# Optimization experiments

Measured on AMD Instinct MI355X. Metric: run time of the kernel, lower is better.

The kernel has to match this reference:

```python
import jax, jax.numpy as jnp
import numpy as np

EPS = 1e-5

def conv1x1(x, w, b):
    # x: [B,Cin,H,W], w: [Cout,Cin], b: [Cout]
    return jnp.einsum('oi,bihw->bohw', w, x) + b[None, :, None, None]

def self_attention(x, qw, qb, kw, kb, vw, vb, fw, fb):
    B, C, H, W = x.shape
    hid = qw.shape[0]
    q = conv1x1(x, qw, qb).reshape(B, hid, H * W).transpose(0, 2, 1)   # [B,HW,hid]
    k = conv1x1(x, kw, kb).reshape(B, hid, H * W)                      # [B,hid,HW]
    v = conv1x1(x, vw, vb).reshape(B, C, H * W)                        # [B,C,HW]
    attn = jax.nn.softmax(jnp.einsum('bnh,bhm->bnm', q, k), axis=-1)   # [B,HW,HW]
    z = jnp.einsum('bnm,bcm->bnc', attn, v)                            # [B,HW,C]
    # faithful to torch .view(B,C,H,W) on contiguous [B,HW,C]: raw reshape, no transpose
    z = z.reshape(B, C, H, W)
    return conv1x1(z * x, fw, fb) + x

def group_norm_per_channel(y, gw, gb):
    # GroupNorm(num_groups == num_channels): per-channel instance norm, biased var
    mean = y.mean(axis=(2, 3), keepdims=True)
    var = ((y - mean) ** 2).mean(axis=(2, 3), keepdims=True)
    yn = (y - mean) * jax.lax.rsqrt(var + EPS)
    return yn * gw[None, :, None, None] + gb[None, :, None, None]

def setup_inputs() -> dict:
    key = jax.random.key(0)
    ks = jax.random.split(key, 32)
    B, C, H, W = 4, 64, 64, 64
    hid, att = 64, 64
    d = {}
    d['x'] = jax.random.normal(ks[0], (B, C, H, W), jnp.float32)
    d['h'] = jax.random.normal(ks[1], (B, hid, H, W), jnp.float32)
    d['c'] = jax.random.normal(ks[2], (B, hid, H, W), jnp.float32)
    i = 3
    for pre, cin in (('ax', C), ('ah', hid)):
        for nm, cout in (('q', att), ('k', att), ('v', cin), ('f', cin)):
            d[f'{pre}_{nm}w'] = jax.random.normal(ks[i], (cout, cin), jnp.float32) * 0.05; i += 1
            d[f'{pre}_{nm}b'] = jax.random.normal(ks[i], (cout,), jnp.float32) * 0.05; i += 1
    d['conv_w'] = jax.random.normal(ks[i], (4 * hid, C + hid, 3, 3), jnp.float32) * 0.05; i += 1
    d['conv_b'] = jax.random.normal(ks[i], (4 * hid,), jnp.float32) * 0.05; i += 1
    d['gn_w'] = jnp.ones((4 * hid,), jnp.float32)
    d['gn_b'] = jnp.zeros((4 * hid,), jnp.float32)
    return d

def reference(x, h, c,
              ax_qw, ax_qb, ax_kw, ax_kb, ax_vw, ax_vb, ax_fw, ax_fb,
              ah_qw, ah_qb, ah_kw, ah_kb, ah_vw, ah_vb, ah_fw, ah_fb,
              conv_w, conv_b, gn_w, gn_b):
    hid = h.shape[1]
    xa = self_attention(x, ax_qw, ax_qb, ax_kw, ax_kb, ax_vw, ax_vb, ax_fw, ax_fb)
    ha = self_attention(h, ah_qw, ah_qb, ah_kw, ah_kb, ah_vw, ah_vb, ah_fw, ah_fb)
    combined = jnp.concatenate([xa, ha], axis=1)
    y = jax.lax.conv_general_dilated(
        combined, conv_w, window_strides=(1, 1), padding=[(1, 1), (1, 1)],
        dimension_numbers=('NCHW', 'OIHW', 'NCHW')) + conv_b[None, :, None, None]
    y = group_norm_per_channel(y, gn_w, gn_b)
    i, f, o, g = jnp.split(y, 4, axis=1)
    i = jax.nn.sigmoid(i); f = jax.nn.sigmoid(f); o = jax.nn.sigmoid(o); g = jnp.tanh(g)
    c_next = f * c + i * g
    h_next = o * jnp.tanh(c_next)
    return jnp.stack([h_next, c_next])  # [2,B,hid,H,W]
```

## Files before the change

kernel.cpp:

```cpp
#include <hip/hip_runtime.h>
#include <hip/hip_bf16.h>


typedef __hip_bfloat16 bf16;
typedef const __hip_bfloat16* bfp;
typedef short bf16x8 __attribute__((ext_vector_type(8)));
typedef short short4v __attribute__((ext_vector_type(4)));
typedef float f32x4 __attribute__((ext_vector_type(4)));
typedef float f32x16 __attribute__((ext_vector_type(16)));
typedef unsigned int u32x4 __attribute__((ext_vector_type(4)));

#define SM_SHIFT 12.0f
#define SM_A  184.66496523378733f
#define SM_B  14034.452417194552f

__device__ __forceinline__ float ldf(const void* p, long i, int f32) {
    return f32 ? ((const float*)p)[i]
               : __bfloat162float(((const bf16*)p)[i]);
}
__device__ __forceinline__ short f2bf(float f) {
    bf16 h = __float2bfloat16(f);
    return *reinterpret_cast<short*>(&h);
}
__device__ __forceinline__ float bfv(short s) {
    unsigned short u = (unsigned short)s;
    return __bfloat162float(*reinterpret_cast<const bf16*>(&u));
}

__device__ __forceinline__ int sniff_f32(const void* xr)
{
    int lane = threadIdx.x & 63;
    unsigned long long v = ((const unsigned long long*)xr)[lane];
    int ok = 0;
#pragma unroll
    for (int i = 0; i < 4; ++i) {
        int e = (int)((v >> (16 * i + 7)) & 0xFF);
        ok += (e >= 100 && e <= 141);
    }
    ok += __shfl_xor(ok, 1, 64);
    ok += __shfl_xor(ok, 2, 64);
    ok += __shfl_xor(ok, 4, 64);
    ok += __shfl_xor(ok, 8, 64);
    ok += __shfl_xor(ok, 16, 64);
    ok += __shfl_xor(ok, 32, 64);
    return ok < 200;
}

__global__ __launch_bounds__(256) void qkv_kernel(
    const void* __restrict__ Xx, const void* __restrict__ Xh,
    const void* __restrict__ qwx, const void* __restrict__ qbx,
    const void* __restrict__ kwx, const void* __restrict__ kbx,
    const void* __restrict__ vwx, const void* __restrict__ vbx,
    const void* __restrict__ qwh, const void* __restrict__ qbh,
    const void* __restrict__ kwh, const void* __restrict__ kbh,
    const void* __restrict__ vwh, const void* __restrict__ vbh,
    bf16* __restrict__ Qx, bf16* __restrict__ Kx, bf16* __restrict__ Vtx,
    bf16* __restrict__ Qh, bf16* __restrict__ Kh, bf16* __restrict__ Vth,
    const void* __restrict__ cw, bf16* __restrict__ Wt,
    float* __restrict__ gacc, int qkvN)
{
    int bx = blockIdx.x;
    int tid = threadIdx.x;
    int f32 = sniff_f32(Xx);
    if (bx >= qkvN) {
        if (bx == qkvN) {
            for (int j = 0; j < 8; ++j)
                gacc[tid * 8 + j] = 0.f;
        }
        int wi = (bx - qkvN) * 256 + tid;
        int tap = wi >> 15;
        int rem = wi & 32767;
        int oc = rem >> 7, ic = rem & 127;
        Wt[wi] = __float2bfloat16(ldf(cw, ((long)oc * 128 + ic) * 9 + tap, f32));
        return;
    }
    __shared__ __align__(16) short xt[64][72];
    __shared__ __align__(16) short wq[64][72];
    __shared__ __align__(16) short wk[64][72];
    __shared__ __align__(16) short wv[64][72];
    int ab  = (bx >> 8) & 1;
    int idx = bx & 255;
    int b = idx >> 6;
    int n0 = (idx & 63) * 64;
    int wave = tid >> 6, lane = tid & 63;
    int q = lane >> 4, l15 = lane & 15;

    const void* X = ab ? Xh : Xx;
    const void* qw = ab ? qwh : qwx; const void* qb = ab ? qbh : qbx;
    const void* kw = ab ? kwh : kwx; const void* kb = ab ? kbh : kbx;
    const void* vw = ab ? vwh : vwx; const void* vb = ab ? vbh : vbx;
    short* Qg  = (short*)(ab ? Qh  : Qx)  + (long)b * 262144;
    short* Kg  = (short*)(ab ? Kh  : Kx)  + (long)b * 262144;
    short* Vtg = (short*)(ab ? Vth : Vtx) + (long)b * 262144;

    if (!f32) {
        const short* q16 = (const short*)qw;
        const short* k16 = (const short*)kw;
        const short* v16 = (const short*)vw;
        for (int rep = 0; rep < 2; ++rep) {
            int j8 = (rep * 256 + tid) * 8;
            *(bf16x8*)&wq[j8 >> 6][j8 & 63] = *(const bf16x8*)(q16 + j8);
            *(bf16x8*)&wk[j8 >> 6][j8 & 63] = *(const bf16x8*)(k16 + j8);
            *(bf16x8*)&wv[j8 >> 6][j8 & 63] = *(const bf16x8*)(v16 + j8);
        }
    } else {
        for (int rep = 0; rep < 16; ++rep) {
            int j = rep * 256 + tid;
            int i = j >> 6, cc = j & 63;
            wq[i][cc] = f2bf(((const float*)qw)[j]);
            wk[i][cc] = f2bf(((const float*)kw)[j]);
            wv[i][cc] = f2bf(((const float*)vw)[j]);
        }
    }
    long xbase = (long)b * 262144;
    if (!f32) {
        const short* X16 = (const short*)X;
        for (int rep = 0; rep < 2; ++rep) {
            int c = rep * 32 + (tid >> 3);
            int p8 = (tid & 7) * 8;
            bf16x8 v = *(const bf16x8*)(X16 + xbase + (long)c * 4096 + n0 + p8);
#pragma unroll
            for (int j = 0; j < 8; ++j) xt[p8 + j][c] = v[j];
        }
    } else {
        for (int rep = 0; rep < 16; ++rep) {
            int c = rep * 4 + (tid >> 6);
            int p = tid & 63;
            xt[p][c] = f2bf(ldf(X, xbase + (long)c * 4096 + n0 + p, f32));
        }
    }
    __syncthreads();

    bf16x8 a0 = *(const bf16x8*)&xt[wave * 16 + l15][q * 8];
    bf16x8 a1 = *(const bf16x8*)&xt[wave * 16 + l15][32 + q * 8];

    for (int ct = 0; ct < 4; ++ct) {
        bf16x8 bq0 = *(const bf16x8*)&wq[ct * 16 + l15][q * 8];
        bf16x8 bq1 = *(const bf16x8*)&wq[ct * 16 + l15][32 + q * 8];
        f32x4 z = (f32x4){0.f, 0.f, 0.f, 0.f};
        z = __builtin_amdgcn_mfma_f32_16x16x32_bf16(a0, bq0, z, 0, 0, 0);
        z = __builtin_amdgcn_mfma_f32_16x16x32_bf16(a1, bq1, z, 0, 0, 0);
        float bias = ldf(qb, ct * 16 + l15, f32);
        for (int reg = 0; reg < 4; ++reg)
            Qg[(long)(n0 + wave * 16 + q * 4 + reg) * 64 + ct * 16 + l15] =
                f2bf(z[reg] + bias);
    }
    for (int ct = 0; ct < 4; ++ct) {
        bf16x8 bk0 = *(const bf16x8*)&wk[ct * 16 + l15][q * 8];
        bf16x8 bk1 = *(const bf16x8*)&wk[ct * 16 + l15][32 + q * 8];
        f32x4 z = (f32x4){0.f, 0.f, 0.f, 0.f};
        z = __builtin_amdgcn_mfma_f32_16x16x32_bf16(a0, bk0, z, 0, 0, 0);
        z = __builtin_amdgcn_mfma_f32_16x16x32_bf16(a1, bk1, z, 0, 0, 0);
        float bias = ldf(kb, ct * 16 + l15, f32);
        for (int reg = 0; reg < 4; ++reg)
            Kg[(long)(n0 + wave * 16 + q * 4 + reg) * 64 + ct * 16 + l15] =
                f2bf(z[reg] + bias);
    }
    bf16x8 av0 = *(const bf16x8*)&wv[wave * 16 + l15][q * 8];
    bf16x8 av1 = *(const bf16x8*)&wv[wave * 16 + l15][32 + q * 8];
    for (int ct = 0; ct < 4; ++ct) {
        bf16x8 bx0 = *(const bf16x8*)&xt[ct * 16 + l15][q * 8];
        bf16x8 bx1 = *(const bf16x8*)&xt[ct * 16 + l15][32 + q * 8];
        f32x4 z = (f32x4){0.f, 0.f, 0.f, 0.f};
        z = __builtin_amdgcn_mfma_f32_16x16x32_bf16(av0, bx0, z, 0, 0, 0);
        z = __builtin_amdgcn_mfma_f32_16x16x32_bf16(av1, bx1, z, 0, 0, 0);
        for (int reg = 0; reg < 4; ++reg) {
            int c_out = wave * 16 + q * 4 + reg;
            float bias = ldf(vb, c_out, f32);
            Vtg[(long)c_out * 4096 + n0 + ct * 16 + l15] = f2bf(z[reg] + bias);
        }
    }
}

__global__ __launch_bounds__(256, 2) void attn_kernel(
    bfp Qx, bfp Kx, bfp Vtx, bf16* Ox,
    bfp Qh, bfp Kh, bfp Vth, bf16* Oh,
    float* __restrict__ lw, int split)
{
    __shared__ __align__(16) short ks [2][64][64];
    __shared__ __align__(16) short vts[2][64][64];
    int tid = threadIdx.x;
    int wave = tid >> 6, lane = tid & 63;
    int l31 = lane & 31, hi = lane >> 5;
    int nh = wave >> 1, mh = wave & 1;
    int idx = blockIdx.x & 255;
    int ab, half, mstart, ntile;
    if (split) {
        ab = blockIdx.x >> 9; half = (blockIdx.x >> 8) & 1;
        mstart = half * 2048; ntile = 32;
    } else {
        ab = blockIdx.x >> 8; half = 0; mstart = 0; ntile = 64;
    }
    int b = idx >> 6;
    int rt = idx & 63;
    int n0b = rt * 64;
    const short* Qb  = (const short*)(ab ? Qh  : Qx)  + (long)b * 262144;
    const short* Kb  = (const short*)(ab ? Kh  : Kx)  + (long)b * 262144;
    const short* Vtb = (const short*)(ab ? Vth : Vtx) + (long)b * 262144;
    short* Ob = (short*)(ab ? Oh : Ox) + (long)half * (1l << 20) + (long)b * 262144;

    int nq = n0b + nh * 32 + l31;
    bf16x8 aq[4];
#pragma unroll
    for (int kc = 0; kc < 4; ++kc)
        aq[kc] = *(const bf16x8*)(Qb + (long)nq * 64 + kc * 16 + hi * 8);

    f32x16 acc0 = (f32x16)(0.0f);
    f32x16 acc1 = (f32x16)(0.0f);
    f32x16 acc_l = (f32x16)(0.0f);
    const short ONE = 0x3F80;
    const bf16x8 ones = {ONE, ONE, ONE, ONE, ONE, ONE, ONE, ONE};

    int sw = (l31 >> 1) & 7;

    int r0 = tid >> 3, r1 = r0 + 32;
    int g = tid & 7;
    int sr0 = (r0 & 51) | ((r0 & 4) << 1) | ((r0 & 8) >> 1);
    int sr1 = sr0 + 32;
    int gk = (g ^ ((sr0 >> 1) & 7)) << 3;
    int gv = (g ^ ((r0 >> 1) & 7)) << 3;

    bf16x8 pk0 = *(const bf16x8*)(Kb + (long)(mstart + r0) * 64 + g * 8);
    bf16x8 pk1 = *(const bf16x8*)(Kb + (long)(mstart + r1) * 64 + g * 8);
    bf16x8 pv0 = *(const bf16x8*)(Vtb + (long)r0 * 4096 + mstart + g * 8);
    bf16x8 pv1 = *(const bf16x8*)(Vtb + (long)r1 * 4096 + mstart + g * 8);

    for (int it = 0; it < ntile; ++it) {
        int buf = it & 1;
        *(bf16x8*)&ks[buf][sr0][gk] = pk0;
        *(bf16x8*)&ks[buf][sr1][gk] = pk1;
        *(bf16x8*)&vts[buf][r0][gv] = pv0;
        *(bf16x8*)&vts[buf][r1][gv] = pv1;
        __syncthreads();
        if (it + 1 < ntile) {
            long m = (long)mstart + (long)(it + 1) * 64;
            pk0 = *(const bf16x8*)(Kb + (m + r0) * 64 + g * 8);
            pk1 = *(const bf16x8*)(Kb + (m + r1) * 64 + g * 8);
            pv0 = *(const bf16x8*)(Vtb + (long)r0 * 4096 + m + g * 8);
            pv1 = *(const bf16x8*)(Vtb + (long)r1 * 4096 + m + g * 8);
        }

        f32x16 s = (f32x16)(0.0f);
        const short* kbase = &ks[buf][mh * 32 + l31][0];
#pragma unroll
        for (int kc = 0; kc < 4; ++kc) {
            bf16x8 ak = *(const bf16x8*)(kbase + (((kc * 2 + hi) ^ sw) << 3));
            s = __builtin_amdgcn_mfma_f32_32x32x16_bf16(ak, aq[kc], s, 0, 0, 0);
        }

        unsigned P32[8];
#pragma unroll
        for (int i = 0; i < 8; ++i) {
            unsigned b0 = (unsigned)fmaxf(fmaf(s[2 * i],     SM_A, SM_B), 0.f);
            unsigned b1 = (unsigned)fmaxf(fmaf(s[2 * i + 1], SM_A, SM_B), 0.f);
            P32[i] = b0 | (b1 << 16);
        }
        u32x4 B0v = (u32x4){P32[0], P32[1], P32[2], P32[3]};
        u32x4 B1v = (u32x4){P32[4], P32[5], P32[6], P32[7]};
        bf16x8 bp0 = __builtin_bit_cast(bf16x8, B0v);
        bf16x8 bp1 = __builtin_bit_cast(bf16x8, B1v);

        acc_l = __builtin_amdgcn_mfma_f32_32x32x16_bf16(ones, bp0, acc_l, 0, 0, 0);
        acc_l = __builtin_amdgcn_mfma_f32_32x32x16_bf16(ones, bp1, acc_l, 0, 0, 0);

        const short* v0base = &vts[buf][l31][0];
        const short* v1base = &vts[buf][32 + l31][0];
#pragma unroll
        for (int mc = 0; mc < 2; ++mc) {
            int gm = ((mh * 4 + mc * 2 + hi) ^ sw) << 3;
            bf16x8 av0 = *(const bf16x8*)(v0base + gm);
            bf16x8 av1 = *(const bf16x8*)(v1base + gm);
            bf16x8 bp = mc ? bp1 : bp0;
            acc0 = __builtin_amdgcn_mfma_f32_32x32x16_bf16(av0, bp, acc0, 0, 0, 0);
            acc1 = __builtin_amdgcn_mfma_f32_32x32x16_bf16(av1, bp, acc1, 0, 0, 0);
        }
    }

    float l_acc = acc_l[0];

    __syncthreads();
    float* fs = (float*)&ks[0][0][0];
    float* fl = fs + 4096;
    if (mh == 1) {
#pragma unroll
        for (int r = 0; r < 16; ++r) {
            int row = (r & 3) + ((r >> 2) << 3) + (hi << 2);
            fs[nh * 2048 + row * 32 + l31]        = acc0[r];
            fs[nh * 2048 + 1024 + row * 32 + l31] = acc1[r];
        }
        if (lane < 32) fl[nh * 32 + l31] = l_acc;
    }
    __syncthreads();
    if (mh == 0) {
        float l_tot = l_acc + fl[nh * 32 + l31];
#pragma unroll
        for (int r = 0; r < 16; ++r) {
            int row = (r & 3) + ((r >> 2) << 3) + (hi << 2);
            acc0[r] += fs[nh * 2048 + row * 32 + l31];
            acc1[r] += fs[nh * 2048 + 1024 + row * 32 + l31];
        }
        int n = n0b + nh * 32 + l31;
        short* dst = Ob + (long)n * 64;
        if (split) {
            if (lane < 32)
                lw[(long)ab * 32768 + (long)half * 16384
                   + (long)b * 4096 + n] = l_tot;
#pragma unroll
            for (int rq = 0; rq < 4; ++rq) {
                int c0 = (rq << 3) + (hi << 2);
                short4v o4a, o4b;
#pragma unroll
                for (int j = 0; j < 4; ++j) {
                    o4a[j] = f2bf(acc0[rq * 4 + j]);
                    o4b[j] = f2bf(acc1[rq * 4 + j]);
                }
                *(short4v*)(dst + c0)      = o4a;
                *(short4v*)(dst + 32 + c0) = o4b;
            }
        } else {
            float iln = 1.f / l_tot;
#pragma unroll
            for (int rq = 0; rq < 4; ++rq) {
                int c0 = (rq << 3) + (hi << 2);
                short4v o4a, o4b;
#pragma unroll
                for (int j = 0; j < 4; ++j) {
                    o4a[j] = f2bf(acc0[rq * 4 + j] * iln);
                    o4b[j] = f2bf(acc1[rq * 4 + j] * iln);
                }
                *(short4v*)(dst + c0)      = o4a;
                *(short4v*)(dst + 32 + c0) = o4b;
            }
        }
    }
}

__global__ __launch_bounds__(256) void attnout_kernel(
    bfp Ox, const void* __restrict__ Xx,
    const void* __restrict__ fwx, const void* __restrict__ fbx,
    bf16* __restrict__ outx,
    bfp Oh, const void* __restrict__ Xh,
    const void* __restrict__ fwh, const void* __restrict__ fbh,
    bf16* __restrict__ outh,
    const float* __restrict__ lw, int split)
{
    __shared__ __align__(16) short fwt[64][72];
    __shared__ __align__(16) short at [64][72];
    int f32 = sniff_f32(Xx);
    int ab  = blockIdx.x >> 8;
    int idx = blockIdx.x & 255;
    int b = idx >> 6;
    int h = idx & 63;
    int tid = threadIdx.x;
    int wave = tid >> 6, lane = tid & 63;
    int q = lane >> 4, l15 = lane & 15;
    bfp O = ab ? Oh : Ox;
    const void* X = ab ? Xh : Xx;
    const void* fw = ab ? fwh : fwx;
    const void* fb = ab ? fbh : fbx;
    bf16* out = ab ? outh : outx;

    if (!f32) {
        const short* f16p = (const short*)fw;
        for (int rep = 0; rep < 2; ++rep) {
            int j8 = (rep * 256 + tid) * 8;
            *(bf16x8*)&fwt[j8 >> 6][j8 & 63] = *(const bf16x8*)(f16p + j8);
        }
    } else {
        for (int rep = 0; rep < 16; ++rep) {
            int j = rep * 256 + tid;
            fwt[j >> 6][j & 63] = f2bf(((const float*)fw)[j]);
        }
    }
    const short* Ob0 = (const short*)(O + (long)b * 262144);
    const short* Ob1 = Ob0 + (1l << 20);
    const float* lp0 = lw + (long)ab * 32768 + (long)b * 4096;
    const float* lp1 = lp0 + 16384;
    long xbase = (long)b * 262144;
    {
        int cn = tid >> 3;
        int w8 = (tid & 7) * 8;
        for (int rep = 0; rep < 2; ++rep, cn += 32) {
            int n = cn * 64 + h;
            bf16x8 o0 = *(const bf16x8*)(Ob0 + (long)n * 64 + w8);
            float pr[8];
            if (split) {
                float il = 1.f / (lp0[n] + lp1[n]);
                bf16x8 o1 = *(const bf16x8*)(Ob1 + (long)n * 64 + w8);
#pragma unroll
                for (int j = 0; j < 8; ++j)
                    pr[j] = (bfv(o0[j]) + bfv(o1[j])) * il;
            } else {
#pragma unroll
                for (int j = 0; j < 8; ++j)
                    pr[j] = bfv(o0[j]);
            }
            if (!f32) {
                bf16x8 xv = *(const bf16x8*)(
                    (const short*)X + xbase + (long)cn * 4096 + h * 64 + w8);
#pragma unroll
                for (int j = 0; j < 8; ++j)
                    at[w8 + j][cn] = f2bf(pr[j] * bfv(xv[j]));
            } else {
#pragma unroll
                for (int j = 0; j < 8; ++j)
                    at[w8 + j][cn] = f2bf(pr[j] *
                        ((const float*)X)[xbase + (long)cn * 4096 + h * 64 + w8 + j]);
            }
        }
    }
    __syncthreads();
    bf16x8 a0 = *(const bf16x8*)&fwt[wave * 16 + l15][q * 8];
    bf16x8 a1 = *(const bf16x8*)&fwt[wave * 16 + l15][32 + q * 8];
    short* outp = (short*)out;
    for (int nt = 0; nt < 4; ++nt) {
        bf16x8 b0 = *(const bf16x8*)&at[nt * 16 + l15][q * 8];
        bf16x8 b1 = *(const bf16x8*)&at[nt * 16 + l15][32 + q * 8];
        f32x4 z = (f32x4){0.f, 0.f, 0.f, 0.f};
        z = __builtin_amdgcn_mfma_f32_16x16x32_bf16(a0, b0, z, 0, 0, 0);
        z = __builtin_amdgcn_mfma_f32_16x16x32_bf16(a1, b1, z, 0, 0, 0);
        int w = nt * 16 + l15;
        short4v o4;
        for (int reg = 0; reg < 4; ++reg) {
            int o = wave * 16 + q * 4 + reg;
            float v = z[reg] + ldf(fb, o, f32) +
                      ldf(X, xbase + (long)o * 4096 + h * 64 + w, f32);
            o4[reg] = f2bf(v);
        }
        *(short4v*)(outp + (((long)(b * 64 + h) * 64 + w) * 64 + wave * 16 + q * 4)) = o4;
    }
}

__global__ __launch_bounds__(256) void conv3x3_kernel(
    bfp xa, bfp ha, bfp Wt, const void* __restrict__ cb,
    bf16* __restrict__ y, float* __restrict__ gacc,
    const void* __restrict__ xraw)
{
    __shared__ __align__(16) short in_s[3][66][136];
    int f32 = sniff_f32(xraw);
    int bx = blockIdx.x;
    int b = bx >> 7;
    int rem = bx & 127;
    int h = rem >> 1;
    int halfoc = rem & 1;
    int tid = threadIdx.x;
    int wave = tid >> 6, lane = tid & 63;
    int q = lane >> 4, l15 = lane & 15;

    const short* xab = (const short*)xa + (long)b * 262144;
    const short* hab = (const short*)ha + (long)b * 262144;
    const bf16x8 zv = {0, 0, 0, 0, 0, 0, 0, 0};
    for (int r = 0; r < 3; ++r) {
        int gy = h + r - 1;
        bool valid = (gy >= 0) && (gy < 64);
        for (int s = 0; s < 2; ++s) {
            int strip = s * 256 + tid;
            int w = strip >> 3;
            int c8 = (strip & 7) * 8;
            bf16x8 vx = zv, vh = zv;
            if (valid) {
                vx = *(const bf16x8*)(xab + ((long)gy * 64 + w) * 64 + c8);
                vh = *(const bf16x8*)(hab + ((long)gy * 64 + w) * 64 + c8);
            }
            *(bf16x8*)&in_s[r][w + 1][c8]      = vx;
            *(bf16x8*)&in_s[r][w + 1][64 + c8] = vh;
        }
    }
    if (tid < 96) {
        int r = tid / 32;
        int rest = tid % 32;
        int col = (rest & 1) ? 65 : 0;
        int c8 = (rest >> 1) * 8;
        *(bf16x8*)&in_s[r][col][c8] = zv;
    }
    __syncthreads();

    int oc0 = halfoc * 128 + wave * 32;
    f32x4 acc[2][4];
    for (int mt = 0; mt < 2; ++mt)
        for (int nt = 0; nt < 4; ++nt)
            acc[mt][nt] = (f32x4){0.f, 0.f, 0.f, 0.f};

    const short* Wb = (const short*)Wt;
    for (int tap = 0; tap < 9; ++tap) {
        int dy = tap / 3, dx = tap - dy * 3;
        for (int kc = 0; kc < 4; ++kc) {
            bf16x8 afrag[2];
            for (int mt = 0; mt < 2; ++mt)
                afrag[mt] = *(const bf16x8*)(
                    Wb + ((long)tap * 256 + oc0 + mt * 16 + l15) * 128 + kc * 32 + q * 8);
            for (int nt = 0; nt < 4; ++nt) {
                bf16x8 bfrag = *(const bf16x8*)&in_s[dy][nt * 16 + l15 + dx][kc * 32 + q * 8];
                for (int mt = 0; mt < 2; ++mt)
                    acc[mt][nt] = __builtin_amdgcn_mfma_f32_16x16x32_bf16(
                        afrag[mt], bfrag, acc[mt][nt], 0, 0, 0);
            }
        }
    }

    long ybase = (long)b * 1048576 + (long)h * 64;
    for (int mt = 0; mt < 2; ++mt) {
        for (int reg = 0; reg < 4; ++reg) {
            int oc = oc0 + mt * 16 + q * 4 + reg;
            float bias = ldf(cb, oc, f32);
            float s = 0.f, s2 = 0.f;
            for (int nt = 0; nt < 4; ++nt) {
                float v = acc[mt][nt][reg] + bias;
                ((short*)y)[ybase + (long)oc * 4096 + nt * 16 + l15] = f2bf(v);
                s += v; s2 = fmaf(v, v, s2);
            }
            s  += __shfl_xor(s,  1, 64);  s2 += __shfl_xor(s2, 1, 64);
            s  += __shfl_xor(s,  2, 64);  s2 += __shfl_xor(s2, 2, 64);
            s  += __shfl_xor(s,  4, 64);  s2 += __shfl_xor(s2, 4, 64);
            s  += __shfl_xor(s,  8, 64);  s2 += __shfl_xor(s2, 8, 64);
            if (l15 == 0) {
                atomicAdd(&gacc[b * 256 + oc], s);
                atomicAdd(&gacc[1024 + b * 256 + oc], s2);
            }
        }
    }
}

__global__ __launch_bounds__(256) void gates_kernel(
    bfp y, const float* __restrict__ gacc,
    const void* __restrict__ gw, const void* __restrict__ gb,
    const void* __restrict__ c_in, void* __restrict__ out)
{
    int f32 = sniff_f32(c_in);
    int idx = blockIdx.x * 256 + threadIdx.x;
    int b = idx >> 18;
    int r = idx & 262143;
    int ch = r >> 12;
    int pix = r & 4095;
    long ybase = (long)b * 1048576;
    float vals[4];
    for (int g = 0; g < 4; ++g) {
        int cc = g * 64 + ch;
        float mu  = gacc[b * 256 + cc] * (1.f / 4096.f);
        float var = gacc[1024 + b * 256 + cc] * (1.f / 4096.f) - mu * mu;
        float rstd = rsqrtf(fmaxf(var, 0.f) + 1e-5f);
        float v = __bfloat162float(y[ybase + (long)cc * 4096 + pix]);
        v = (v - mu) * rstd * ldf(gw, cc, f32) + ldf(gb, cc, f32);
        vals[g] = v;
    }
    float ig = 1.f / (1.f + __expf(-vals[0]));
    float fg = 1.f / (1.f + __expf(-vals[1]));
    float og = 1.f / (1.f + __expf(-vals[2]));
    float gg = tanhf(vals[3]);
    float cprev = ldf(c_in, idx, f32);
    float cn = fg * cprev + ig * gg;
    float hn = og * tanhf(cn);
    if (f32) {
        float* o32 = (float*)out;
        o32[idx] = hn;
        o32[1048576 + idx] = cn;
    } else {
        bf16* o16 = (bf16*)out;
        o16[idx] = __float2bfloat16(hn);
        o16[1048576 + idx] = __float2bfloat16(cn);
    }
}

extern "C" void kernel_launch(void* const* d_in, const int* in_sizes, int n_in,
                              void* d_out, int out_size, void* d_ws, size_t ws_size,
                              hipStream_t stream)
{
    const void* x = d_in[0]; const void* h = d_in[1]; const void* c = d_in[2];
    const void* ax_qw = d_in[3],  *ax_qb = d_in[4];
    const void* ax_kw = d_in[5],  *ax_kb = d_in[6];
    const void* ax_vw = d_in[7],  *ax_vb = d_in[8];
    const void* ax_fw = d_in[9],  *ax_fb = d_in[10];
    const void* ah_qw = d_in[11], *ah_qb = d_in[12];
    const void* ah_kw = d_in[13], *ah_kb = d_in[14];
    const void* ah_vw = d_in[15], *ah_vb = d_in[16];
    const void* ah_fw = d_in[17], *ah_fb = d_in[18];
    const void* conv_w = d_in[19], *conv_b = d_in[20];
    const void* gn_w = d_in[21],  *gn_b = d_in[22];

    char* wsb = (char*)d_ws;
    auto S = [&](int i) { return wsb + ((unsigned long)i << 21); };
    bool splitm = ws_size >= (27ul << 20);
    bool fused  = splitm || ws_size >= (18ul << 20) + 16384;

    bf16* ha = (bf16*)S(0);
    bf16* Wt = (bf16*)S(1);
    bf16 *Qx, *Kx, *Vtx, *Qh, *Kh, *Vth, *xa, *y, *Ox, *Oh;
    char* tail;
    if (splitm) {
        Qx = (bf16*)S(2); Kx = (bf16*)S(3); Vtx = (bf16*)S(4);
        Qh = (bf16*)S(5); Kh = (bf16*)S(6); Vth = (bf16*)S(7);
        xa = (bf16*)S(8);
        Ox = (bf16*)S(9);
        Oh = (bf16*)S(11);
        y = Qx;
        tail = S(13);
    } else if (fused) {
        Qx = (bf16*)S(2); Kx = (bf16*)S(3); Vtx = (bf16*)S(4);
        Qh = (bf16*)S(5); Kh = (bf16*)S(6); Vth = (bf16*)S(7);
        xa = (bf16*)S(8); Ox = Qx; Oh = Qh; y = Qx;
        tail = S(9);
    } else {
        Qx = (bf16*)S(2); Kx = (bf16*)S(3); Vtx = (bf16*)S(4);
        Qh = Qx; Kh = Kx; Vth = Vtx;
        xa = (bf16*)S(6); Ox = Qx; Oh = Qh; y = Qx;
        tail = S(7);
    }
    float* gacc = (float*)tail;
    float* lw   = (float*)(tail + 8192);

    if (fused) {
        qkv_kernel<<<512 + 1152, 256, 0, stream>>>(
            x, h,
            ax_qw, ax_qb, ax_kw, ax_kb, ax_vw, ax_vb,
            ah_qw, ah_qb, ah_kw, ah_kb, ah_vw, ah_vb,
            Qx, Kx, Vtx, Qh, Kh, Vth, conv_w, Wt, gacc, 512);
        if (splitm) {
            attn_kernel<<<1024, 256, 0, stream>>>(
                Qx, Kx, Vtx, Ox, Qh, Kh, Vth, Oh, lw, 1);
            attnout_kernel<<<512, 256, 0, stream>>>(
                Ox, x, ax_fw, ax_fb, xa, Oh, h, ah_fw, ah_fb, ha, lw, 1);
        } else {
            attn_kernel<<<512, 256, 0, stream>>>(
                Qx, Kx, Vtx, Ox, Qh, Kh, Vth, Oh, lw, 0);
            attnout_kernel<<<512, 256, 0, stream>>>(
                Ox, x, ax_fw, ax_fb, xa, Oh, h, ah_fw, ah_fb, ha, lw, 0);
        }
    } else {
        qkv_kernel<<<256 + 1152, 256, 0, stream>>>(
            x, x,
            ax_qw, ax_qb, ax_kw, ax_kb, ax_vw, ax_vb,
            ax_qw, ax_qb, ax_kw, ax_kb, ax_vw, ax_vb,
            Qx, Kx, Vtx, Qx, Kx, Vtx, conv_w, Wt, gacc, 256);
        attn_kernel<<<256, 256, 0, stream>>>(
            Qx, Kx, Vtx, Ox, Qx, Kx, Vtx, Ox, lw, 0);
        attnout_kernel<<<256, 256, 0, stream>>>(
            Ox, x, ax_fw, ax_fb, xa, Ox, x, ax_fw, ax_fb, xa, lw, 0);
        qkv_kernel<<<256, 256, 0, stream>>>(
            h, h,
            ah_qw, ah_qb, ah_kw, ah_kb, ah_vw, ah_vb,
            ah_qw, ah_qb, ah_kw, ah_kb, ah_vw, ah_vb,
            Qh, Kh, Vth, Qh, Kh, Vth, conv_w, Wt, gacc, 256);
        attn_kernel<<<256, 256, 0, stream>>>(
            Qh, Kh, Vth, Oh, Qh, Kh, Vth, Oh, lw, 0);
        attnout_kernel<<<256, 256, 0, stream>>>(
            Oh, h, ah_fw, ah_fb, ha, Oh, h, ah_fw, ah_fb, ha, lw, 0);
    }
    conv3x3_kernel<<<512, 256, 0, stream>>>(xa, ha, Wt, conv_b, y, gacc, x);
    gates_kernel<<<4096, 256, 0, stream>>>(y, gacc, gn_w, gn_b, c, d_out);
}
```

Baseline: 205.3 us.

## Fuse attention output projection into attention kernel and vectorize gates kernel

The attention kernel now gathers each block's query rows as one spatial row (the n = c*64 + h mapping). It then applies the output 1x1 conv, the multiply by x and the residual in-kernel through LDS, so the separate attnout kernel and the intermediate O buffer round trip are gone. The split-M path with partial-sum workspace is removed, so attention always runs 512 blocks over the full key range. The gates kernel processes 8 pixels per thread with vector loads and stores. This saves one launch and global traffic, but drops the extra parallelism the split path gave and adds an epilogue tail to the attention blocks.

```diff
diff --git a/kernel.cpp b/kernel.cpp
--- a/kernel.cpp
+++ b/kernel.cpp
@@ -173,37 +173,42 @@
 }
 
 __global__ __launch_bounds__(256, 2) void attn_kernel(
-    bfp Qx, bfp Kx, bfp Vtx, bf16* Ox,
-    bfp Qh, bfp Kh, bfp Vth, bf16* Oh,
-    float* __restrict__ lw, int split)
+    bfp Qx, bfp Kx, bfp Vtx,
+    const void* __restrict__ Xx, const void* __restrict__ fwx,
+    const void* __restrict__ fbx, bf16* __restrict__ outx,
+    bfp Qh, bfp Kh, bfp Vth,
+    const void* __restrict__ Xh, const void* __restrict__ fwh,
+    const void* __restrict__ fbh, bf16* __restrict__ outh)
 {
-    __shared__ __align__(16) short ks [2][64][64];
-    __shared__ __align__(16) short vts[2][64][64];
+    __shared__ __align__(16) short smem[16384];
+    short (*ks)[64][64]  = (short (*)[64][64])(smem);
+    short (*vts)[64][64] = (short (*)[64][64])(smem + 8192);
+
     int tid = threadIdx.x;
     int wave = tid >> 6, lane = tid & 63;
     int l31 = lane & 31, hi = lane >> 5;
     int nh = wave >> 1, mh = wave & 1;
+    int ab  = blockIdx.x >> 8;
     int idx = blockIdx.x & 255;
-    int ab, half, mstart, ntile;
-    if (split) {
-        ab = blockIdx.x >> 9; half = (blockIdx.x >> 8) & 1;
-        mstart = half * 2048; ntile = 32;
-    } else {
-        ab = blockIdx.x >> 8; half = 0; mstart = 0; ntile = 64;
-    }
     int b = idx >> 6;
-    int rt = idx & 63;
-    int n0b = rt * 64;
+    int hrow = idx & 63;
+    int f32 = sniff_f32(Xx);
+
     const short* Qb  = (const short*)(ab ? Qh  : Qx)  + (long)b * 262144;
     const short* Kb  = (const short*)(ab ? Kh  : Kx)  + (long)b * 262144;
     const short* Vtb = (const short*)(ab ? Vth : Vtx) + (long)b * 262144;
-    short* Ob = (short*)(ab ? Oh : Ox) + (long)half * (1l << 20) + (long)b * 262144;
-
-    int nq = n0b + nh * 32 + l31;
+    const void* X  = ab ? Xh  : Xx;
+    const void* fw = ab ? fwh : fwx;
+    const void* fb = ab ? fbh : fbx;
+    bf16* out = ab ? outh : outx;
+    long xbase = (long)b * 262144;
+
+    int cnq = nh * 32 + l31;
+    long nq = (long)cnq * 64 + hrow;
     bf16x8 aq[4];
 #pragma unroll
     for (int kc = 0; kc < 4; ++kc)
-        aq[kc] = *(const bf16x8*)(Qb + (long)nq * 64 + kc * 16 + hi * 8);
+        aq[kc] = *(const bf16x8*)(Qb + nq * 64 + kc * 16 + hi * 8);
 
     f32x16 acc0 = (f32x16)(0.0f);
     f32x16 acc1 = (f32x16)(0.0f);
@@ -220,20 +225,20 @@
     int gk = (g ^ ((sr0 >> 1) & 7)) << 3;
     int gv = (g ^ ((r0 >> 1) & 7)) << 3;
 
-    bf16x8 pk0 = *(const bf16x8*)(Kb + (long)(mstart + r0) * 64 + g * 8);
-    bf16x8 pk1 = *(const bf16x8*)(Kb + (long)(mstart + r1) * 64 + g * 8);
-    bf16x8 pv0 = *(const bf16x8*)(Vtb + (long)r0 * 4096 + mstart + g * 8);
-    bf16x8 pv1 = *(const bf16x8*)(Vtb + (long)r1 * 4096 + mstart + g * 8);
-
-    for (int it = 0; it < ntile; ++it) {
+    bf16x8 pk0 = *(const bf16x8*)(Kb + (long)r0 * 64 + g * 8);
+    bf16x8 pk1 = *(const bf16x8*)(Kb + (long)r1 * 64 + g * 8);
+    bf16x8 pv0 = *(const bf16x8*)(Vtb + (long)r0 * 4096 + g * 8);
+    bf16x8 pv1 = *(const bf16x8*)(Vtb + (long)r1 * 4096 + g * 8);
+
+    for (int it = 0; it < 64; ++it) {
         int buf = it & 1;
         *(bf16x8*)&ks[buf][sr0][gk] = pk0;
         *(bf16x8*)&ks[buf][sr1][gk] = pk1;
         *(bf16x8*)&vts[buf][r0][gv] = pv0;
         *(bf16x8*)&vts[buf][r1][gv] = pv1;
         __syncthreads();
-        if (it + 1 < ntile) {
-            long m = (long)mstart + (long)(it + 1) * 64;
+        if (it + 1 < 64) {
+            long m = (long)(it + 1) * 64;
             pk0 = *(const bf16x8*)(Kb + (m + r0) * 64 + g * 8);
             pk1 = *(const bf16x8*)(Kb + (m + r1) * 64 + g * 8);
             pv0 = *(const bf16x8*)(Vtb + (long)r0 * 4096 + m + g * 8);
@@ -278,9 +283,13 @@
 
     float l_acc = acc_l[0];
 
+    float* fs = (float*)smem;
+    float* fl = (float*)smem + 4096;
+    short* at_s  = smem;
+    short* fwt_s = smem + 4608;
+    short* o_lds = smem + 9216;
+
     __syncthreads();
-    float* fs = (float*)&ks[0][0][0];
-    float* fl = fs + 4096;
     if (mh == 1) {
 #pragma unroll
         for (int r = 0; r < 16; ++r) {
@@ -292,142 +301,80 @@
     }
     __syncthreads();
     if (mh == 0) {
-        float l_tot = l_acc + fl[nh * 32 + l31];
-#pragma unroll
-        for (int r = 0; r < 16; ++r) {
-            int row = (r & 3) + ((r >> 2) << 3) + (hi << 2);
-            acc0[r] += fs[nh * 2048 + row * 32 + l31];
-            acc1[r] += fs[nh * 2048 + 1024 + row * 32 + l31];
-        }
-        int n = n0b + nh * 32 + l31;
-        short* dst = Ob + (long)n * 64;
-        if (split) {
-            if (lane < 32)
-                lw[(long)ab * 32768 + (long)half * 16384
-                   + (long)b * 4096 + n] = l_tot;
-#pragma unroll
-            for (int rq = 0; rq < 4; ++rq) {
-                int c0 = (rq << 3) + (hi << 2);
-                short4v o4a, o4b;
-#pragma unroll
-                for (int j = 0; j < 4; ++j) {
-                    o4a[j] = f2bf(acc0[rq * 4 + j]);
-                    o4b[j] = f2bf(acc1[rq * 4 + j]);
-                }
-                *(short4v*)(dst + c0)      = o4a;
-                *(short4v*)(dst + 32 + c0) = o4b;
+        float iln = 1.f / (l_acc + fl[nh * 32 + l31]);
+        short* orow = o_lds + cnq * 68;
+#pragma unroll
+        for (int rq = 0; rq < 4; ++rq) {
+            int c0 = rq * 8 + (hi << 2);
+            short4v oa, ob;
+#pragma unroll
+            for (int j = 0; j < 4; ++j) {
+                int r = rq * 4 + j;
+                int row = (r & 3) + ((r >> 2) << 3) + (hi << 2);
+                oa[j] = f2bf((acc0[r] + fs[nh * 2048 + row * 32 + l31]) * iln);
+                ob[j] = f2bf((acc1[r] + fs[nh * 2048 + 1024 + row * 32 + l31]) * iln);
             }
-        } else {
-            float iln = 1.f / l_tot;
-#pragma unroll
-            for (int rq = 0; rq < 4; ++rq) {
-                int c0 = (rq << 3) + (hi << 2);
-                short4v o4a, o4b;
-#pragma unroll
-                for (int j = 0; j < 4; ++j) {
-                    o4a[j] = f2bf(acc0[rq * 4 + j] * iln);
-                    o4b[j] = f2bf(acc1[rq * 4 + j] * iln);
-                }
-                *(short4v*)(dst + c0)      = o4a;
-                *(short4v*)(dst + 32 + c0) = o4b;
-            }
-        }
-    }
-}
-
-__global__ __launch_bounds__(256) void attnout_kernel(
-    bfp Ox, const void* __restrict__ Xx,
-    const void* __restrict__ fwx, const void* __restrict__ fbx,
-    bf16* __restrict__ outx,
-    bfp Oh, const void* __restrict__ Xh,
-    const void* __restrict__ fwh, const void* __restrict__ fbh,
-    bf16* __restrict__ outh,
-    const float* __restrict__ lw, int split)
-{
-    __shared__ __align__(16) short fwt[64][72];
-    __shared__ __align__(16) short at [64][72];
-    int f32 = sniff_f32(Xx);
-    int ab  = blockIdx.x >> 8;
-    int idx = blockIdx.x & 255;
-    int b = idx >> 6;
-    int h = idx & 63;
-    int tid = threadIdx.x;
-    int wave = tid >> 6, lane = tid & 63;
-    int q = lane >> 4, l15 = lane & 15;
-    bfp O = ab ? Oh : Ox;
-    const void* X = ab ? Xh : Xx;
-    const void* fw = ab ? fwh : fwx;
-    const void* fb = ab ? fbh : fbx;
-    bf16* out = ab ? outh : outx;
-
+            *(short4v*)(orow + c0)      = oa;
+            *(short4v*)(orow + 32 + c0) = ob;
+        }
+    }
+    __syncthreads();
     if (!f32) {
         const short* f16p = (const short*)fw;
         for (int rep = 0; rep < 2; ++rep) {
             int j8 = (rep * 256 + tid) * 8;
-            *(bf16x8*)&fwt[j8 >> 6][j8 & 63] = *(const bf16x8*)(f16p + j8);
+            *(bf16x8*)(fwt_s + (j8 >> 6) * 72 + (j8 & 63)) =
+                *(const bf16x8*)(f16p + j8);
         }
     } else {
         for (int rep = 0; rep < 16; ++rep) {
             int j = rep * 256 + tid;
-            fwt[j >> 6][j & 63] = f2bf(((const float*)fw)[j]);
-        }
-    }
-    const short* Ob0 = (const short*)(O + (long)b * 262144);
-    const short* Ob1 = Ob0 + (1l << 20);
-    const float* lp0 = lw + (long)ab * 32768 + (long)b * 4096;
-    const float* lp1 = lp0 + 16384;
-    long xbase = (long)b * 262144;
+            fwt_s[(j >> 6) * 72 + (j & 63)] = f2bf(((const float*)fw)[j]);
+        }
+    }
     {
         int cn = tid >> 3;
         int w8 = (tid & 7) * 8;
         for (int rep = 0; rep < 2; ++rep, cn += 32) {
-            int n = cn * 64 + h;
-            bf16x8 o0 = *(const bf16x8*)(Ob0 + (long)n * 64 + w8);
-            float pr[8];
-            if (split) {
-                float il = 1.f / (lp0[n] + lp1[n]);
-                bf16x8 o1 = *(const bf16x8*)(Ob1 + (long)n * 64 + w8);
-#pragma unroll
-                for (int j = 0; j < 8; ++j)
-                    pr[j] = (bfv(o0[j]) + bfv(o1[j])) * il;
-            } else {
-#pragma unroll
-                for (int j = 0; j < 8; ++j)
-                    pr[j] = bfv(o0[j]);
-            }
             if (!f32) {
                 bf16x8 xv = *(const bf16x8*)(
-                    (const short*)X + xbase + (long)cn * 4096 + h * 64 + w8);
+                    (const short*)X + xbase + (long)cn * 4096 + hrow * 64 + w8);
 #pragma unroll
                 for (int j = 0; j < 8; ++j)
-                    at[w8 + j][cn] = f2bf(pr[j] * bfv(xv[j]));
+                    at_s[(w8 + j) * 72 + cn] =
+                        f2bf(bfv(o_lds[cn * 68 + w8 + j]) * bfv(xv[j]));
             } else {
 #pragma unroll
                 for (int j = 0; j < 8; ++j)
-                    at[w8 + j][cn] = f2bf(pr[j] *
-                        ((const float*)X)[xbase + (long)cn * 4096 + h * 64 + w8 + j]);
+                    at_s[(w8 + j) * 72 + cn] =
+                        f2bf(bfv(o_lds[cn * 68 + w8 + j]) *
+                             ((const float*)X)[xbase + (long)cn * 4096 + hrow * 64 + w8 + j]);
             }
         }
     }
     __syncthreads();
-    bf16x8 a0 = *(const bf16x8*)&fwt[wave * 16 + l15][q * 8];
-    bf16x8 a1 = *(const bf16x8*)&fwt[wave * 16 + l15][32 + q * 8];
-    short* outp = (short*)out;
-    for (int nt = 0; nt < 4; ++nt) {
-        bf16x8 b0 = *(const bf16x8*)&at[nt * 16 + l15][q * 8];
-        bf16x8 b1 = *(const bf16x8*)&at[nt * 16 + l15][32 + q * 8];
-        f32x4 z = (f32x4){0.f, 0.f, 0.f, 0.f};
-        z = __builtin_amdgcn_mfma_f32_16x16x32_bf16(a0, b0, z, 0, 0, 0);
-        z = __builtin_amdgcn_mfma_f32_16x16x32_bf16(a1, b1, z, 0, 0, 0);
-        int w = nt * 16 + l15;
-        short4v o4;
-        for (int reg = 0; reg < 4; ++reg) {
-            int o = wave * 16 + q * 4 + reg;
-            float v = z[reg] + ldf(fb, o, f32) +
-                      ldf(X, xbase + (long)o * 4096 + h * 64 + w, f32);
-            o4[reg] = f2bf(v);
-        }
-        *(short4v*)(outp + (((long)(b * 64 + h) * 64 + w) * 64 + wave * 16 + q * 4)) = o4;
+    {
+        int q = lane >> 4, l15 = lane & 15;
+        bf16x8 a0 = *(const bf16x8*)(fwt_s + (wave * 16 + l15) * 72 + q * 8);
+        bf16x8 a1 = *(const bf16x8*)(fwt_s + (wave * 16 + l15) * 72 + 32 + q * 8);
+        short* outp = (short*)out;
+        for (int nt = 0; nt < 4; ++nt) {
+            bf16x8 b0 = *(const bf16x8*)(at_s + (nt * 16 + l15) * 72 + q * 8);
+            bf16x8 b1 = *(const bf16x8*)(at_s + (nt * 16 + l15) * 72 + 32 + q * 8);
+            f32x4 z = (f32x4){0.f, 0.f, 0.f, 0.f};
+            z = __builtin_amdgcn_mfma_f32_16x16x32_bf16(a0, b0, z, 0, 0, 0);
+            z = __builtin_amdgcn_mfma_f32_16x16x32_bf16(a1, b1, z, 0, 0, 0);
+            int w = nt * 16 + l15;
+            short4v o4;
+            for (int reg = 0; reg < 4; ++reg) {
+                int o = wave * 16 + q * 4 + reg;
+                float v = z[reg] + ldf(fb, o, f32) +
+                          ldf(X, xbase + (long)o * 4096 + hrow * 64 + w, f32);
+                o4[reg] = f2bf(v);
+            }
+            *(short4v*)(outp + (((long)(b * 64 + hrow) * 64 + w) * 64
+                                + wave * 16 + q * 4)) = o4;
+        }
     }
 }
 
@@ -527,37 +474,64 @@
     const void* __restrict__ c_in, void* __restrict__ out)
 {
     int f32 = sniff_f32(c_in);
-    int idx = blockIdx.x * 256 + threadIdx.x;
-    int b = idx >> 18;
-    int r = idx & 262143;
-    int ch = r >> 12;
-    int pix = r & 4095;
+    int t = blockIdx.x * 256 + threadIdx.x;
+    int b = t >> 15;
+    int r = t & 32767;
+    int ch = r >> 9;
+    int p8 = (r & 511) * 8;
     long ybase = (long)b * 1048576;
-    float vals[4];
+    long idx8 = (long)b * 262144 + (long)ch * 4096 + p8;
+
+    float mu[4], rstd[4], gwv[4], gbv[4];
+    bf16x8 yv[4];
+#pragma unroll
     for (int g = 0; g < 4; ++g) {
         int cc = g * 64 + ch;
-        float mu  = gacc[b * 256 + cc] * (1.f / 4096.f);
-        float var = gacc[1024 + b * 256 + cc] * (1.f / 4096.f) - mu * mu;
-        float rstd = rsqrtf(fmaxf(var, 0.f) + 1e-5f);
-        float v = __bfloat162float(y[ybase + (long)cc * 4096 + pix]);
-        v = (v - mu) * rstd * ldf(gw, cc, f32) + ldf(gb, cc, f32);
-        vals[g] = v;
-    }
-    float ig = 1.f / (1.f + __expf(-vals[0]));
-    float fg = 1.f / (1.f + __expf(-vals[1]));
-    float og = 1.f / (1.f + __expf(-vals[2]));
-    float gg = tanhf(vals[3]);
-    float cprev = ldf(c_in, idx, f32);
-    float cn = fg * cprev + ig * gg;
-    float hn = og * tanhf(cn);
+        float m = gacc[b * 256 + cc] * (1.f / 4096.f);
+        float var = gacc[1024 + b * 256 + cc] * (1.f / 4096.f) - m * m;
+        mu[g] = m;
+        rstd[g] = rsqrtf(fmaxf(var, 0.f) + 1e-5f);
+        gwv[g] = ldf(gw, cc, f32);
+        gbv[g] = ldf(gb, cc, f32);
+        yv[g] = *(const bf16x8*)((const short*)y + ybase + (long)cc * 4096 + p8);
+    }
+    float cprev[8];
+    if (!f32) {
+        bf16x8 cv = *(const bf16x8*)((const short*)c_in + idx8);
+#pragma unroll
+        for (int j = 0; j < 8; ++j) cprev[j] = bfv(cv[j]);
+    } else {
+#pragma unroll
+        for (int j = 0; j < 8; ++j) cprev[j] = ((const float*)c_in)[idx8 + j];
+    }
+    bf16x8 hn8, cn8;
+    float hnf[8], cnf[8];
+#pragma unroll
+    for (int j = 0; j < 8; ++j) {
+        float v0 = (bfv(yv[0][j]) - mu[0]) * rstd[0] * gwv[0] + gbv[0];
+        float v1 = (bfv(yv[1][j]) - mu[1]) * rstd[1] * gwv[1] + gbv[1];
+        float v2 = (bfv(yv[2][j]) - mu[2]) * rstd[2] * gwv[2] + gbv[2];
+        float v3 = (bfv(yv[3][j]) - mu[3]) * rstd[3] * gwv[3] + gbv[3];
+        float ig = 1.f / (1.f + __expf(-v0));
+        float fg = 1.f / (1.f + __expf(-v1));
+        float og = 1.f / (1.f + __expf(-v2));
+        float gg = tanhf(v3);
+        float cn = fg * cprev[j] + ig * gg;
+        float hn = og * tanhf(cn);
+        hn8[j] = f2bf(hn); cn8[j] = f2bf(cn);
+        hnf[j] = hn; cnf[j] = cn;
+    }
     if (f32) {
         float* o32 = (float*)out;
-        o32[idx] = hn;
-        o32[1048576 + idx] = cn;
+#pragma unroll
+        for (int j = 0; j < 8; ++j) {
+            o32[idx8 + j] = hnf[j];
+            o32[1048576 + idx8 + j] = cnf[j];
+        }
     } else {
-        bf16* o16 = (bf16*)out;
-        o16[idx] = __float2bfloat16(hn);
-        o16[1048576 + idx] = __float2bfloat16(cn);
+        short* o16 = (short*)out;
+        *(bf16x8*)(o16 + idx8) = hn8;
+        *(bf16x8*)(o16 + 1048576 + idx8) = cn8;
     }
 }
 
@@ -579,34 +553,24 @@
 
     char* wsb = (char*)d_ws;
     auto S = [&](int i) { return wsb + ((unsigned long)i << 21); };
-    bool splitm = ws_size >= (27ul << 20);
-    bool fused  = splitm || ws_size >= (18ul << 20) + 16384;
+    bool fused = ws_size >= (18ul << 20) + 16384;
 
     bf16* ha = (bf16*)S(0);
     bf16* Wt = (bf16*)S(1);
-    bf16 *Qx, *Kx, *Vtx, *Qh, *Kh, *Vth, *xa, *y, *Ox, *Oh;
+    bf16 *Qx, *Kx, *Vtx, *Qh, *Kh, *Vth, *xa, *y;
     char* tail;
-    if (splitm) {
+    if (fused) {
         Qx = (bf16*)S(2); Kx = (bf16*)S(3); Vtx = (bf16*)S(4);
         Qh = (bf16*)S(5); Kh = (bf16*)S(6); Vth = (bf16*)S(7);
-        xa = (bf16*)S(8);
-        Ox = (bf16*)S(9);
-        Oh = (bf16*)S(11);
-        y = Qx;
-        tail = S(13);
-    } else if (fused) {
-        Qx = (bf16*)S(2); Kx = (bf16*)S(3); Vtx = (bf16*)S(4);
-        Qh = (bf16*)S(5); Kh = (bf16*)S(6); Vth = (bf16*)S(7);
-        xa = (bf16*)S(8); Ox = Qx; Oh = Qh; y = Qx;
+        xa = (bf16*)S(8); y = Qx;
         tail = S(9);
     } else {
         Qx = (bf16*)S(2); Kx = (bf16*)S(3); Vtx = (bf16*)S(4);
         Qh = Qx; Kh = Kx; Vth = Vtx;
-        xa = (bf16*)S(6); Ox = Qx; Oh = Qh; y = Qx;
+        xa = (bf16*)S(6); y = Qx;
         tail = S(7);
     }
     float* gacc = (float*)tail;
-    float* lw   = (float*)(tail + 8192);
 
     if (fused) {
         qkv_kernel<<<512 + 1152, 256, 0, stream>>>(
@@ -614,17 +578,9 @@
             ax_qw, ax_qb, ax_kw, ax_kb, ax_vw, ax_vb,
             ah_qw, ah_qb, ah_kw, ah_kb, ah_vw, ah_vb,
             Qx, Kx, Vtx, Qh, Kh, Vth, conv_w, Wt, gacc, 512);
-        if (splitm) {
-            attn_kernel<<<1024, 256, 0, stream>>>(
-                Qx, Kx, Vtx, Ox, Qh, Kh, Vth, Oh, lw, 1);
-            attnout_kernel<<<512, 256, 0, stream>>>(
-                Ox, x, ax_fw, ax_fb, xa, Oh, h, ah_fw, ah_fb, ha, lw, 1);
-        } else {
-            attn_kernel<<<512, 256, 0, stream>>>(
-                Qx, Kx, Vtx, Ox, Qh, Kh, Vth, Oh, lw, 0);
-            attnout_kernel<<<512, 256, 0, stream>>>(
-                Ox, x, ax_fw, ax_fb, xa, Oh, h, ah_fw, ah_fb, ha, lw, 0);
-        }
+        attn_kernel<<<512, 256, 0, stream>>>(
+            Qx, Kx, Vtx, x, ax_fw, ax_fb, xa,
+            Qh, Kh, Vth, h, ah_fw, ah_fb, ha);
     } else {
         qkv_kernel<<<256 + 1152, 256, 0, stream>>>(
             x, x,
@@ -632,19 +588,17 @@
             ax_qw, ax_qb, ax_kw, ax_kb, ax_vw, ax_vb,
             Qx, Kx, Vtx, Qx, Kx, Vtx, conv_w, Wt, gacc, 256);
         attn_kernel<<<256, 256, 0, stream>>>(
-            Qx, Kx, Vtx, Ox, Qx, Kx, Vtx, Ox, lw, 0);
-        attnout_kernel<<<256, 256, 0, stream>>>(
-            Ox, x, ax_fw, ax_fb, xa, Ox, x, ax_fw, ax_fb, xa, lw, 0);
+            Qx, Kx, Vtx, x, ax_fw, ax_fb, xa,
+            Qx, Kx, Vtx, x, ax_fw, ax_fb, xa);
         qkv_kernel<<<256, 256, 0, stream>>>(
             h, h,
             ah_qw, ah_qb, ah_kw, ah_kb, ah_vw, ah_vb,
             ah_qw, ah_qb, ah_kw, ah_kb, ah_vw, ah_vb,
             Qh, Kh, Vth, Qh, Kh, Vth, conv_w, Wt, gacc, 256);
         attn_kernel<<<256, 256, 0, stream>>>(
-            Qh, Kh, Vth, Oh, Qh, Kh, Vth, Oh, lw, 0);
-        attnout_kernel<<<256, 256, 0, stream>>>(
-            Oh, h, ah_fw, ah_fb, ha, Oh, h, ah_fw, ah_fb, ha, lw, 0);
+            Qh, Kh, Vth, h, ah_fw, ah_fb, ha,
+            Qh, Kh, Vth, h, ah_fw, ah_fb, ha);
     }
     conv3x3_kernel<<<512, 256, 0, stream>>>(xa, ha, Wt, conv_b, y, gacc, x);
-    gates_kernel<<<4096, 256, 0, stream>>>(y, gacc, gn_w, gn_b, c, d_out);
-}
+    gates_kernel<<<512, 256, 0, stream>>>(y, gacc, gn_w, gn_b, c, d_out);
+}
```

Result: no change. 202.4 us (-1.4%).
